# Optimization experiments

Measured on AMD Instinct MI355X. Metric: run time of the kernel, lower is better.

Reference implementation:

```python
import jax, jax.numpy as jnp
import numpy as np

MAX_DISP = 64


def setup_inputs() -> dict:
    key = jax.random.key(0)
    k1, k2 = jax.random.split(key)
    b, c, h, w = 4, 256, 180, 320
    left_feature = jax.random.normal(k1, (b, c, h, w), dtype=jnp.float32)
    right_feature = jax.random.normal(k2, (b, c, h, w), dtype=jnp.float32)
    return {"left_feature": left_feature, "right_feature": right_feature}


def reference(left_feature, right_feature):
    # Correlation cost volume: cost[:, i, :, x] = mean_c(left[:, :, :, x] * right[:, :, :, x - i])
    # for x >= i, else 0. Loop is over the small fixed disparity range (init arg).
    b, c, h, w = left_feature.shape
    slices = []
    for i in range(MAX_DISP):
        if i > 0:
            prod = jnp.mean(left_feature[:, :, :, i:] * right_feature[:, :, :, :-i], axis=1)  # [b, h, w-i]
            prod = jnp.pad(prod, ((0, 0), (0, 0), (i, 0)))  # zero-fill columns < i
        else:
            prod = jnp.mean(left_feature * right_feature, axis=1)  # [b, h, w]
        slices.append(prod)
    cost_volume = jnp.stack(slices, axis=1)  # [b, max_disp, h, w]
    return cost_volume
```

## Files before the change

### kernel.cpp

```cpp
#include <hip/hip_runtime.h>


typedef short bf16x8 __attribute__((ext_vector_type(8)));
typedef float f32x4 __attribute__((ext_vector_type(4)));

#define Bb 4
#define Cc 256
#define Hh 180
#define Ww 320
#define MAXD 64
#define KC 32
#define NCHUNK (Cc / KC)
#define RSTR 20
#define HW (Hh * Ww)
#define LROWS 160
#define RROWS 224

__device__ __forceinline__ unsigned int bf16rne2(float a, float b) {
    unsigned int ua = __float_as_uint(a);
    unsigned int ub = __float_as_uint(b);
    ua = (ua + 0x7FFFu + ((ua >> 16) & 1u)) >> 16;
    ub = (ub + 0x7FFFu + ((ub >> 16) & 1u)) & 0xFFFF0000u;
    return ua | ub;
}

__global__ __launch_bounds__(320, 4)
void _AA_CostVolume_63668595196248_kernel(const float* __restrict__ L,
                                          const float* __restrict__ R,
                                          float* __restrict__ out) {
    __shared__ unsigned int sL[LROWS * RSTR];
    __shared__ unsigned int sR[RROWS * RSTR];

    const int tid = threadIdx.x;
    const int bi  = blockIdx.x;
    const int xh  = bi & 1;
    const int rid = bi >> 1;
    const int b   = rid / Hh;
    const int h   = rid % Hh;
    const int X0  = xh * 160;

    if (xh == 0) {
        const int ob = (b * MAXD * Hh + h) * Ww;
        for (int z = tid; z < MAXD * MAXD; z += 320) {
            const int i = z >> 6;
            const int x = z & 63;
            if (x < i) out[ob + i * HW + x] = 0.0f;
        }
    }

    const int lane = tid & 63;
    const int w    = tid >> 6;
    const int q    = lane >> 4;
    const int n    = lane & 15;

    const int cp = tid & 15;
    const int tq = tid >> 4;

    const float* baseL = L + (b * Cc + 2 * cp) * HW + h * Ww + X0;
    const float* baseR = R + (b * Cc + 2 * cp) * HW + h * Ww + X0 - 64;

    const bool rv0 = (xh != 0) || (tq >= 16);
    const bool rv2 = (tq < 16);

    const int frag_off = n * RSTR + 4 * q;
    const int luMin = (xh == 0) ? 4 : 0;

    f32x4 acc[2][5];
#pragma unroll
    for (int xt = 0; xt < 2; ++xt)
#pragma unroll
        for (int du = 0; du < 5; ++du) {
            f32x4 z = {0.f, 0.f, 0.f, 0.f};
            acc[xt][du] = z;
        }

    float4 pl0a, pl0b, pl1a, pl1b;
    float4 pr0a, pr0b, pr1a, pr1b, pr2a, pr2b;

#define LOADCHUNK(KCI) do {                                               \
        const int ko = (KCI) * (KC * HW);                                 \
        pl0a = *(const float4*)(baseL + ko + 4 * tq);                     \
        pl0b = *(const float4*)(baseL + ko + HW + 4 * tq);                \
        pl1a = *(const float4*)(baseL + ko + 4 * (tq + 20));              \
        pl1b = *(const float4*)(baseL + ko + HW + 4 * (tq + 20));         \
        if (rv0) {                                                       \
            pr0a = *(const float4*)(baseR + ko + 4 * tq);                 \
            pr0b = *(const float4*)(baseR + ko + HW + 4 * tq);            \
        }                                                                \
        pr1a = *(const float4*)(baseR + ko + 4 * (tq + 20));              \
        pr1b = *(const float4*)(baseR + ko + HW + 4 * (tq + 20));         \
        if (rv2) {                                                       \
            pr2a = *(const float4*)(baseR + ko + 4 * (tq + 40));          \
            pr2b = *(const float4*)(baseR + ko + HW + 4 * (tq + 40));     \
        }                                                                \
    } while (0)

#define STORE4(SBUF, ROW0, VA, VB) do {                                   \
        const float* _fa = (const float*)&(VA);                           \
        const float* _fb = (const float*)&(VB);                           \
        _Pragma("unroll")                                                 \
        for (int j = 0; j < 4; ++j)                                       \
            SBUF[((ROW0) + j) * RSTR + cp] = bf16rne2(_fa[j], _fb[j]);    \
    } while (0)

    LOADCHUNK(0);

    for (int kc = 0; kc < NCHUNK; ++kc) {
        __syncthreads();
        STORE4(sL, 4 * tq, pl0a, pl0b);
        STORE4(sL, 4 * (tq + 20), pl1a, pl1b);
        if (rv0) STORE4(sR, 4 * tq, pr0a, pr0b);
        STORE4(sR, 4 * (tq + 20), pr1a, pr1b);
        if (rv2) STORE4(sR, 4 * (tq + 40), pr2a, pr2b);
        __syncthreads();

        if (kc + 1 < NCHUNK) LOADCHUNK(kc + 1);

        const bf16x8 af0 = *(const bf16x8*)&sL[(16 * (2 * w + 0) + n) * RSTR + 4 * q];
        const bf16x8 af1 = *(const bf16x8*)&sL[(16 * (2 * w + 1) + n) * RSTR + 4 * q];

#pragma unroll
        for (int uu = 0; uu < 6; ++uu) {
            const int lu = 2 * w + uu;
            if (lu >= luMin) {
                const bf16x8 bfr = *(const bf16x8*)&sR[lu * (16 * RSTR) + frag_off];
                if (uu <= 4)
                    acc[0][4 - uu] = __builtin_amdgcn_mfma_f32_16x16x32_bf16(
                        af0, bfr, acc[0][4 - uu], 0, 0, 0);
                if (uu >= 1)
                    acc[1][5 - uu] = __builtin_amdgcn_mfma_f32_16x16x32_bf16(
                        af1, bfr, acc[1][5 - uu], 0, 0, 0);
            }
        }
    }

    const float sc = 1.0f / 256.0f;
#pragma unroll
    for (int xt = 0; xt < 2; ++xt) {
        const int gt = 10 * xh + 2 * w + xt;
        const int x0 = 16 * gt + 4 * q;
#pragma unroll
        for (int du = 0; du < 5; ++du) {
            if (gt - du >= 0) {
                const int ib = 16 * du + 4 * q - n;
#pragma unroll
                for (int r = 0; r < 4; ++r) {
                    const int i = ib + r;
                    if (i >= 0 && i < MAXD)
                        out[((b * MAXD + i) * Hh + h) * Ww + x0 + r] = acc[xt][du][r] * sc;
                }
            }
        }
    }
#undef LOADCHUNK
#undef STORE4
}

extern "C" void kernel_launch(void* const* d_in, const int* in_sizes, int n_in,
                              void* d_out, int out_size, void* d_ws, size_t ws_size,
                              hipStream_t stream) {
    const float* left  = (const float*)d_in[0];
    const float* right = (const float*)d_in[1];
    float* out = (float*)d_out;
    dim3 grid(2 * Bb * Hh);
    dim3 block(320);
    _AA_CostVolume_63668595196248_kernel<<<grid, block, 0, stream>>>(left, right, out);
}
```

Before: 508.0 us.

## Transpose shared-memory layout for vector stores and stage output through LDS

Each thread now packs two channels into 128-bit LDS stores: shared rows are indexed by channel pair and columns by x position, with padded strides. MFMA fragments are therefore read as four scalar LDS loads instead of one vector load. The epilogue stages the accumulators in shared memory, two halves of 32 disparities at a time, then writes full float4 rows of the output. This replaces scattered 4-byte global stores with coalesced 16-byte stores. In exchange it adds extra barriers, more fragment-read instructions per chunk, and global loads partitioned differently across threads.

New measurement: 497.8 us. -2.0%, faster.

```diff
diff --git a/kernel.cpp b/kernel.cpp
--- a/kernel.cpp
+++ b/kernel.cpp
@@ -11,10 +11,10 @@
 #define MAXD 64
 #define KC 32
 #define NCHUNK (Cc / KC)
-#define RSTR 20
 #define HW (Hh * Ww)
-#define LROWS 160
-#define RROWS 224
+#define LSTR 164
+#define RSTR2 228
+#define EST 164
 
 __device__ __forceinline__ unsigned int bf16rne2(float a, float b) {
     unsigned int ua = __float_as_uint(a);
@@ -24,12 +24,22 @@
     return ua | ub;
 }
 
+__device__ __forceinline__ bf16x8 frag_read(const unsigned int* s, int stride,
+                                            int q, int col) {
+    union { unsigned int d[4]; bf16x8 v; } u;
+#pragma unroll
+    for (int jj = 0; jj < 4; ++jj) u.d[jj] = s[(4 * q + jj) * stride + col];
+    return u.v;
+}
+
 __global__ __launch_bounds__(320, 4)
 void _AA_CostVolume_63668595196248_kernel(const float* __restrict__ L,
                                           const float* __restrict__ R,
                                           float* __restrict__ out) {
-    __shared__ unsigned int sL[LROWS * RSTR];
-    __shared__ unsigned int sR[RROWS * RSTR];
+    __shared__ unsigned int smem[6272];
+    unsigned int* sL = smem;
+    unsigned int* sR = smem + 16 * LSTR;
+    float* eps = (float*)smem;
 
     const int tid = threadIdx.x;
     const int bi  = blockIdx.x;
@@ -53,16 +63,28 @@
     const int q    = lane >> 4;
     const int n    = lane & 15;
 
-    const int cp = tid & 15;
-    const int tq = tid >> 4;
-
-    const float* baseL = L + (b * Cc + 2 * cp) * HW + h * Ww + X0;
-    const float* baseR = R + (b * Cc + 2 * cp) * HW + h * Ww + X0 - 64;
-
-    const bool rv0 = (xh != 0) || (tq >= 16);
-    const bool rv2 = (tq < 16);
-
-    const int frag_off = n * RSTR + 4 * q;
+    const int cpL = tid / 40;
+    const int xqL = tid % 40;
+    const int cpR0 = tid / 56;
+    const int fR0  = tid % 56;
+    const int cpR1 = (tid + 320) / 56;
+    const int fR1  = (tid + 320) % 56;
+    const int cpR2 = (tid + 640) / 56;
+    const int fR2  = (tid + 640) % 56;
+
+    const float* Lbase = L + (b * Cc) * HW + h * Ww + X0;
+    const float* Rbase = R + (b * Cc) * HW + h * Ww + X0 - 64;
+
+    const bool rvg0 = (xh != 0) || (fR0 >= 16);
+    const bool rvg1 = (xh != 0) || (fR1 >= 16);
+    const bool rvg2 = (tid < 256) && ((xh != 0) || (fR2 >= 16));
+
+    const int wL0 = cpL * LSTR + 4 * xqL;
+    const int wL1 = (cpL + 8) * LSTR + 4 * xqL;
+    const int wR0 = cpR0 * RSTR2 + 4 * fR0;
+    const int wR1 = cpR1 * RSTR2 + 4 * fR1;
+    const int wR2 = cpR2 * RSTR2 + 4 * fR2;
+
     const int luMin = (xh == 0) ? 4 : 0;
 
     f32x4 acc[2][5];
@@ -74,56 +96,61 @@
             acc[xt][du] = z;
         }
 
-    float4 pl0a, pl0b, pl1a, pl1b;
-    float4 pr0a, pr0b, pr1a, pr1b, pr2a, pr2b;
-
-#define LOADCHUNK(KCI) do {                                               \
-        const int ko = (KCI) * (KC * HW);                                 \
-        pl0a = *(const float4*)(baseL + ko + 4 * tq);                     \
-        pl0b = *(const float4*)(baseL + ko + HW + 4 * tq);                \
-        pl1a = *(const float4*)(baseL + ko + 4 * (tq + 20));              \
-        pl1b = *(const float4*)(baseL + ko + HW + 4 * (tq + 20));         \
-        if (rv0) {                                                       \
-            pr0a = *(const float4*)(baseR + ko + 4 * tq);                 \
-            pr0b = *(const float4*)(baseR + ko + HW + 4 * tq);            \
-        }                                                                \
-        pr1a = *(const float4*)(baseR + ko + 4 * (tq + 20));              \
-        pr1b = *(const float4*)(baseR + ko + HW + 4 * (tq + 20));         \
-        if (rv2) {                                                       \
-            pr2a = *(const float4*)(baseR + ko + 4 * (tq + 40));          \
-            pr2b = *(const float4*)(baseR + ko + HW + 4 * (tq + 40));     \
-        }                                                                \
+    float4 pl0a = {0,0,0,0}, pl0b = {0,0,0,0}, pl1a = {0,0,0,0}, pl1b = {0,0,0,0};
+    float4 pr0a = {0,0,0,0}, pr0b = {0,0,0,0}, pr1a = {0,0,0,0}, pr1b = {0,0,0,0};
+    float4 pr2a = {0,0,0,0}, pr2b = {0,0,0,0};
+
+#define LOADCHUNK(KCI) do {                                                  \
+        const float* Lc = Lbase + (KCI) * (KC * HW);                         \
+        const float* Rc = Rbase + (KCI) * (KC * HW);                         \
+        pl0a = *(const float4*)(Lc + (2 * cpL) * HW + 4 * xqL);              \
+        pl0b = *(const float4*)(Lc + (2 * cpL + 1) * HW + 4 * xqL);          \
+        pl1a = *(const float4*)(Lc + (2 * cpL + 16) * HW + 4 * xqL);         \
+        pl1b = *(const float4*)(Lc + (2 * cpL + 17) * HW + 4 * xqL);         \
+        if (rvg0) {                                                          \
+            pr0a = *(const float4*)(Rc + (2 * cpR0) * HW + 4 * fR0);         \
+            pr0b = *(const float4*)(Rc + (2 * cpR0 + 1) * HW + 4 * fR0);     \
+        }                                                                    \
+        if (rvg1) {                                                          \
+            pr1a = *(const float4*)(Rc + (2 * cpR1) * HW + 4 * fR1);         \
+            pr1b = *(const float4*)(Rc + (2 * cpR1 + 1) * HW + 4 * fR1);     \
+        }                                                                    \
+        if (rvg2) {                                                          \
+            pr2a = *(const float4*)(Rc + (2 * cpR2) * HW + 4 * fR2);         \
+            pr2b = *(const float4*)(Rc + (2 * cpR2 + 1) * HW + 4 * fR2);     \
+        }                                                                    \
     } while (0)
 
-#define STORE4(SBUF, ROW0, VA, VB) do {                                   \
-        const float* _fa = (const float*)&(VA);                           \
-        const float* _fb = (const float*)&(VB);                           \
-        _Pragma("unroll")                                                 \
-        for (int j = 0; j < 4; ++j)                                       \
-            SBUF[((ROW0) + j) * RSTR + cp] = bf16rne2(_fa[j], _fb[j]);    \
+#define PACKST(SBUF, WOFF, VA, VB) do {                                      \
+        union { unsigned int d[4]; uint4 v4; } _u;                           \
+        _u.d[0] = bf16rne2((VA).x, (VB).x);                                  \
+        _u.d[1] = bf16rne2((VA).y, (VB).y);                                  \
+        _u.d[2] = bf16rne2((VA).z, (VB).z);                                  \
+        _u.d[3] = bf16rne2((VA).w, (VB).w);                                  \
+        *(uint4*)&SBUF[WOFF] = _u.v4;                                        \
     } while (0)
 
     LOADCHUNK(0);
 
     for (int kc = 0; kc < NCHUNK; ++kc) {
         __syncthreads();
-        STORE4(sL, 4 * tq, pl0a, pl0b);
-        STORE4(sL, 4 * (tq + 20), pl1a, pl1b);
-        if (rv0) STORE4(sR, 4 * tq, pr0a, pr0b);
-        STORE4(sR, 4 * (tq + 20), pr1a, pr1b);
-        if (rv2) STORE4(sR, 4 * (tq + 40), pr2a, pr2b);
+        PACKST(sL, wL0, pl0a, pl0b);
+        PACKST(sL, wL1, pl1a, pl1b);
+        if (rvg0) PACKST(sR, wR0, pr0a, pr0b);
+        if (rvg1) PACKST(sR, wR1, pr1a, pr1b);
+        if (rvg2) PACKST(sR, wR2, pr2a, pr2b);
         __syncthreads();
 
         if (kc + 1 < NCHUNK) LOADCHUNK(kc + 1);
 
-        const bf16x8 af0 = *(const bf16x8*)&sL[(16 * (2 * w + 0) + n) * RSTR + 4 * q];
-        const bf16x8 af1 = *(const bf16x8*)&sL[(16 * (2 * w + 1) + n) * RSTR + 4 * q];
+        const bf16x8 af0 = frag_read(sL, LSTR, q, 16 * (2 * w + 0) + n);
+        const bf16x8 af1 = frag_read(sL, LSTR, q, 16 * (2 * w + 1) + n);
 
 #pragma unroll
         for (int uu = 0; uu < 6; ++uu) {
             const int lu = 2 * w + uu;
             if (lu >= luMin) {
-                const bf16x8 bfr = *(const bf16x8*)&sR[lu * (16 * RSTR) + frag_off];
+                const bf16x8 bfr = frag_read(sR, RSTR2, q, 16 * lu + n);
                 if (uu <= 4)
                     acc[0][4 - uu] = __builtin_amdgcn_mfma_f32_16x16x32_bf16(
                         af0, bfr, acc[0][4 - uu], 0, 0, 0);
@@ -135,25 +162,49 @@
     }
 
     const float sc = 1.0f / 256.0f;
-#pragma unroll
-    for (int xt = 0; xt < 2; ++xt) {
-        const int gt = 10 * xh + 2 * w + xt;
-        const int x0 = 16 * gt + 4 * q;
-#pragma unroll
-        for (int du = 0; du < 5; ++du) {
-            if (gt - du >= 0) {
-                const int ib = 16 * du + 4 * q - n;
-#pragma unroll
-                for (int r = 0; r < 4; ++r) {
-                    const int i = ib + r;
-                    if (i >= 0 && i < MAXD)
-                        out[((b * MAXD + i) * Hh + h) * Ww + x0 + r] = acc[xt][du][r] * sc;
+    const int til = tid / 40;
+    const int fd  = tid % 40;
+
+    for (int ihalf = 0; ihalf < 2; ++ihalf) {
+        __syncthreads();
+        const int ilo = 32 * ihalf;
+#pragma unroll
+        for (int xt = 0; xt < 2; ++xt) {
+            const int lt = 2 * w + xt;
+            const int gt = 10 * xh + lt;
+#pragma unroll
+            for (int du = 0; du < 5; ++du) {
+                if (gt - du >= 0) {
+                    const int ib = 16 * du + 4 * q - n;
+#pragma unroll
+                    for (int r = 0; r < 4; ++r) {
+                        const int i = ib + r;
+                        if (i >= ilo && i < ilo + 32)
+                            eps[(i - ilo) * EST + 16 * lt + 4 * q + r] =
+                                acc[xt][du][r] * sc;
+                    }
                 }
             }
         }
+        __syncthreads();
+#pragma unroll
+        for (int p = 0; p < 4; ++p) {
+            const int il = 8 * p + til;
+            const int i  = ilo + il;
+            const float4 v = *(const float4*)&eps[il * EST + 4 * fd];
+            float* op = out + ((b * MAXD + i) * Hh + h) * Ww + X0 + 4 * fd;
+            if (xh || 4 * fd >= i) {
+                *(float4*)op = v;
+            } else {
+                const float* vf = (const float*)&v;
+#pragma unroll
+                for (int e = 0; e < 4; ++e)
+                    if (4 * fd + e >= i) op[e] = vf[e];
+            }
+        }
     }
 #undef LOADCHUNK
-#undef STORE4
+#undef PACKST
 }
 
 extern "C" void kernel_launch(void* const* d_in, const int* in_sizes, int n_in,
```
